# Kernel optimization log

Measured on AMD Instinct MI355X. Metric: run time of the kernel, lower is better.

## Reference

```python
import jax, jax.numpy as jnp
import numpy as np

B, T, H = 262144, 15, 64


def setup_inputs() -> dict:
    key = jax.random.key(0)
    ks = jax.random.split(key, 8)
    s_ih = 1.0 / np.sqrt(H)
    return {
        "x": jax.random.normal(ks[0], (B, T), dtype=jnp.float32),
        # PyTorch GRU params: W_ih [3H, input_size=1], W_hh [3H, H], biases [3H]
        "W_ih": jax.random.uniform(ks[1], (3 * H, 1), jnp.float32, -s_ih, s_ih),
        "W_hh": jax.random.uniform(ks[2], (3 * H, H), jnp.float32, -s_ih, s_ih),
        "b_ih": jax.random.uniform(ks[3], (3 * H,), jnp.float32, -s_ih, s_ih),
        "b_hh": jax.random.uniform(ks[4], (3 * H,), jnp.float32, -s_ih, s_ih),
        "W_fc": jax.random.uniform(ks[5], (2, H), jnp.float32, -s_ih, s_ih),
        "b_fc": jax.random.uniform(ks[6], (2,), jnp.float32, -s_ih, s_ih),
    }


def reference(x, W_ih, W_hh, b_ih, b_hh, W_fc, b_fc):
    # x: [B, T]; each scalar feature is one timestep of a 1-dim GRU input.
    w_in = W_ih[:, 0]  # [3H] since input_size == 1

    def step(h, x_t):
        # x_t: [B]; input gates are just outer product with w_in (input_size=1)
        xg = x_t[:, None] * w_in[None, :] + b_ih          # [B, 3H]
        hg = h @ W_hh.T + b_hh                            # [B, 3H]
        r = jax.nn.sigmoid(xg[:, :H] + hg[:, :H])
        z = jax.nn.sigmoid(xg[:, H:2 * H] + hg[:, H:2 * H])
        n = jnp.tanh(xg[:, 2 * H:] + r * hg[:, 2 * H:])
        h_new = (1.0 - z) * n + z * h
        return h_new, None

    h0 = jnp.zeros((x.shape[0], H), dtype=x.dtype)
    h_last, _ = jax.lax.scan(step, h0, x.T)  # scan over time dim
    logits = h_last @ W_fc.T + b_fc          # [B, 2]
    return logits
```

## Files before the change

kernel.cpp:

```cpp
#include <hip/hip_runtime.h>

#define T_STEPS 15
#define ROWS_PER_BLOCK 64
#define B_TOTAL 262144
#define LOG2E 1.4426950408889634f

typedef _Float16 half8 __attribute__((ext_vector_type(8)));
typedef _Float16 half4 __attribute__((ext_vector_type(4)));
typedef __fp16   fp16x2 __attribute__((ext_vector_type(2)));
typedef float f32x4 __attribute__((ext_vector_type(4)));

#define MFMA_INIT(acc, a, b, cseed) \
    asm("v_mfma_f32_16x16x32_f16 %0, %1, %2, %3" : "=&v"(acc) : "v"(a), "v"(b), "v"(cseed))
#define MFMA_ACC(acc, a, b) \
    asm("v_mfma_f32_16x16x32_f16 %0, %1, %2, %0" : "+v"(acc) : "v"(a), "v"(b))

__device__ __forceinline__ int swz(int row, int e) {
    return (row * 64 + e) ^ ((row & 7) << 3);
}

__global__ __launch_bounds__(256, 3) void gru_mfma_kernel(
    const float* __restrict__ x,
    const float* __restrict__ W_ih,
    const float* __restrict__ W_hh,
    const float* __restrict__ b_ih,
    const float* __restrict__ b_hh,
    const float* __restrict__ W_fc,
    const float* __restrict__ b_fc,
    float* __restrict__ out)
{
    __shared__ _Float16 wlds[192 * 64];
    __shared__ float    xlds[T_STEPS * ROWS_PER_BLOCK];
    __shared__ _Float16 hst[4][2][16 * 64];

    const int tid  = threadIdx.x;
    const int wave = tid >> 6;
    const int lane = tid & 63;
    const int c    = lane & 15;
    const int g4   = lane >> 4;
    const int r0   = blockIdx.x * ROWS_PER_BLOCK;

    for (int idx = tid; idx < 192 * 64; idx += 256) {
        int n = idx >> 6, s = idx & 63;
        int korig = (s & 3) * 16 + (s >> 2);
        float scale = (n < 128) ? LOG2E : (2.0f * LOG2E);
        wlds[swz(n, s)] = (_Float16)(W_hh[n * 64 + korig] * scale);
    }
    for (int idx = tid; idx < ROWS_PER_BLOCK * T_STEPS; idx += 256) {
        int row = idx / T_STEPS, t = idx - row * T_STEPS;
        xlds[t * 64 + row] = x[r0 * T_STEPS + idx];
    }
    __syncthreads();

    float wihr[4], wihz[4], wihn[4], seedn[4], bihn[4];
    f32x4 sr4[4], sz4[4];
#pragma unroll
    for (int tq = 0; tq < 4; ++tq) {
        int jn = tq * 16 + c;
        wihr[tq]  = W_ih[jn] * LOG2E;
        wihz[tq]  = W_ih[64 + jn] * LOG2E;
        wihn[tq]  = W_ih[128 + jn] * (2.0f * LOG2E);
        float sr  = (b_ih[jn] + b_hh[jn]) * LOG2E;
        float sz  = (b_ih[64 + jn] + b_hh[64 + jn]) * LOG2E;
        sr4[tq] = (f32x4){sr, sr, sr, sr};
        sz4[tq] = (f32x4){sz, sz, sz, sz};
        seedn[tq] = b_hh[128 + jn] * (2.0f * LOG2E);
        bihn[tq]  = b_ih[128 + jn] * (2.0f * LOG2E);
    }

    const int eS0 = c * 64 + (((g4 * 8) + 0)  ^ ((c & 7) << 3));
    const int eS1 = c * 64 + (((g4 * 8) + 32) ^ ((c & 7) << 3));
    const int bytesS0 = eS0 * 2;
    const int bytesS1 = eS1 * 2;
    const _Float16* aptr0 = &hst[wave][0][eS0];
    const _Float16* aptr1 = &hst[wave][0][eS1];
    _Float16* wr[4];
#pragma unroll
    for (int reg = 0; reg < 4; ++reg) {
        int row = g4 * 4 + reg;
        wr[reg] = &hst[wave][0][row * 64 + ((c * 4) ^ ((row & 7) << 3))];
    }

    const f32x4 zero4 = (f32x4){0.0f, 0.0f, 0.0f, 0.0f};

    f32x4 accr[4], accz[4], accn[4];
#pragma unroll
    for (int tq = 0; tq < 4; ++tq) {
        accr[tq] = sr4[tq];
        accz[tq] = sz4[tq];
        accn[tq] = zero4;
    }

    float h[4][4];
#pragma unroll
    for (int tq = 0; tq < 4; ++tq)
#pragma unroll
        for (int reg = 0; reg < 4; ++reg) h[tq][reg] = 0.0f;

    const char* wbase = (const char*)&wlds[0];

#pragma unroll 1
    for (int t = 0; t < T_STEPS; ++t) {
        if (t > 0) {
            int ofA = bytesS0, ofB = bytesS1;
            asm volatile("" : "+v"(ofA), "+v"(ofB));
            const char* bp0 = wbase + ofA;
            const char* bp1 = wbase + ofB;

            half8 Ahi0 = *(const half8*)aptr0;
            half8 Ahi1 = *(const half8*)aptr1;
            half8 Alo0 = *(const half8*)(aptr0 + 1024);
            half8 Alo1 = *(const half8*)(aptr1 + 1024);
#pragma unroll
            for (int tq = 0; tq < 4; ++tq) {
                half8 Br0 = *(const half8*)(bp0 + tq * 2048);
                half8 Br1 = *(const half8*)(bp1 + tq * 2048);
                half8 Bz0 = *(const half8*)(bp0 + (4 + tq) * 2048);
                half8 Bz1 = *(const half8*)(bp1 + (4 + tq) * 2048);
                half8 Bn0 = *(const half8*)(bp0 + (8 + tq) * 2048);
                half8 Bn1 = *(const half8*)(bp1 + (8 + tq) * 2048);
                MFMA_INIT(accr[tq], Ahi0, Br0, sr4[tq]);
                MFMA_ACC (accr[tq], Ahi1, Br1);
                MFMA_INIT(accz[tq], Ahi0, Bz0, sz4[tq]);
                MFMA_ACC (accz[tq], Ahi1, Bz1);
                MFMA_INIT(accn[tq], Ahi0, Bn0, zero4);
                MFMA_ACC (accn[tq], Ahi1, Bn1);
                MFMA_ACC (accn[tq], Alo0, Bn0);
                MFMA_ACC (accn[tq], Alo1, Bn1);
                if (tq < 3) __builtin_amdgcn_sched_barrier(0);
            }
            __builtin_amdgcn_sched_barrier(0);
            asm volatile("s_nop 7\n\ts_nop 7");
            __builtin_amdgcn_sched_barrier(0);
        }

        f32x4 xt4 = *(const f32x4*)&xlds[t * 64 + wave * 16 + g4 * 4];

#pragma unroll
        for (int reg = 0; reg < 4; ++reg) {
            float xt = xt4[reg];
            float hnv[4];
#pragma unroll
            for (int tq = 0; tq < 4; ++tq) {
                float pr = __builtin_fmaf(xt, wihr[tq], accr[tq][reg]);
                float er = __builtin_amdgcn_exp2f(-pr);
                float rg = __builtin_amdgcn_rcpf(1.0f + er);
                float pz = __builtin_fmaf(xt, wihz[tq], accz[tq][reg]);
                float ez = __builtin_amdgcn_exp2f(-pz);
                float na2 = __builtin_fmaf(rg, seedn[tq],
                             __builtin_fmaf(xt, wihn[tq], bihn[tq]));
                float na  = __builtin_fmaf(rg, accn[tq][reg], na2);
                float en = __builtin_amdgcn_exp2f(-na);
                float A  = 1.0f + en;
                float Cc = 1.0f + ez;
                float D  = A * Cc;
                float R  = __builtin_amdgcn_rcpf(D);
                float P  = __builtin_fmaf(-en, ez, ez);
                float num = __builtin_fmaf(h[tq][reg], A, P);
                float hn = num * R;
                h[tq][reg] = hn;
                hnv[tq] = hn;
            }
            fp16x2 h01 = __builtin_amdgcn_cvt_pkrtz(hnv[0], hnv[1]);
            fp16x2 h23 = __builtin_amdgcn_cvt_pkrtz(hnv[2], hnv[3]);
            float l0 = hnv[0] - (float)h01[0];
            float l1 = hnv[1] - (float)h01[1];
            float l2 = hnv[2] - (float)h23[0];
            float l3 = hnv[3] - (float)h23[1];
            fp16x2 l01 = __builtin_amdgcn_cvt_pkrtz(l0, l1);
            fp16x2 l23 = __builtin_amdgcn_cvt_pkrtz(l2, l3);
            half4 vh, vl;
            vh[0] = (_Float16)h01[0]; vh[1] = (_Float16)h01[1];
            vh[2] = (_Float16)h23[0]; vh[3] = (_Float16)h23[1];
            vl[0] = (_Float16)l01[0]; vl[1] = (_Float16)l01[1];
            vl[2] = (_Float16)l23[0]; vl[3] = (_Float16)l23[1];
            *(half4*)wr[reg] = vh;
            *(half4*)(wr[reg] + 1024) = vl;
        }
    }

    const float* wfc = W_fc;
    const float* bfc = b_fc;
    asm volatile("" : "+v"(wfc), "+v"(bfc));
    float wfc0[4], wfc1[4];
#pragma unroll
    for (int tq = 0; tq < 4; ++tq) {
        wfc0[tq] = wfc[tq * 16 + c];
        wfc1[tq] = wfc[64 + tq * 16 + c];
    }
#pragma unroll
    for (int reg = 0; reg < 4; ++reg) {
        float s0 = 0.0f, s1 = 0.0f;
#pragma unroll
        for (int tq = 0; tq < 4; ++tq) {
            s0 = __builtin_fmaf(h[tq][reg], wfc0[tq], s0);
            s1 = __builtin_fmaf(h[tq][reg], wfc1[tq], s1);
        }
#pragma unroll
        for (int m = 1; m < 16; m <<= 1) {
            s0 += __shfl_xor(s0, m, 64);
            s1 += __shfl_xor(s1, m, 64);
        }
        if (c == 0) {
            int gr = r0 + wave * 16 + g4 * 4 + reg;
            out[gr * 2 + 0] = s0 + bfc[0];
            out[gr * 2 + 1] = s1 + bfc[1];
        }
    }
}

extern "C" void kernel_launch(void* const* d_in, const int* in_sizes, int n_in,
                              void* d_out, int out_size, void* d_ws, size_t ws_size,
                              hipStream_t stream) {
    const float* x    = (const float*)d_in[0];
    const float* W_ih = (const float*)d_in[1];
    const float* W_hh = (const float*)d_in[2];
    const float* b_ih = (const float*)d_in[3];
    const float* b_hh = (const float*)d_in[4];
    const float* W_fc = (const float*)d_in[5];
    const float* b_fc = (const float*)d_in[6];
    float* out = (float*)d_out;

    dim3 grid(B_TOTAL / ROWS_PER_BLOCK);
    dim3 block(256);
    gru_mfma_kernel<<<grid, block, 0, stream>>>(x, W_ih, W_hh, b_ih, b_hh, W_fc, b_fc, out);
}
```

Baseline: 236.2 us.

## Drop fp16 hi/lo split of hidden state and process two row tiles per wave

Removes the low-part correction for the hidden state, so h is stored in LDS as a single fp16 value and the n-gate no longer needs two extra MFMAs. Each wave now handles two 16-row tiles, with 128 rows per block, so the W_hh B-fragments loaded from LDS are reused across both tiles. Biases are added in the scalar epilogue instead of seeding the MFMA accumulators. Occupancy drops from 3 to 2 blocks per CU, and the lower-precision recurrence may lose accuracy against the fp32 reference.

```diff
diff --git a/kernel.cpp b/kernel.cpp
--- a/kernel.cpp
+++ b/kernel.cpp
@@ -1,7 +1,7 @@
 #include <hip/hip_runtime.h>
 
 #define T_STEPS 15
-#define ROWS_PER_BLOCK 64
+#define ROWS_PER_BLOCK 128
 #define B_TOTAL 262144
 #define LOG2E 1.4426950408889634f
 
@@ -10,8 +10,8 @@
 typedef __fp16   fp16x2 __attribute__((ext_vector_type(2)));
 typedef float f32x4 __attribute__((ext_vector_type(4)));
 
-#define MFMA_INIT(acc, a, b, cseed) \
-    asm("v_mfma_f32_16x16x32_f16 %0, %1, %2, %3" : "=&v"(acc) : "v"(a), "v"(b), "v"(cseed))
+#define MFMA_INIT(acc, a, b, cz) \
+    asm("v_mfma_f32_16x16x32_f16 %0, %1, %2, %3" : "=&v"(acc) : "v"(a), "v"(b), "v"(cz))
 #define MFMA_ACC(acc, a, b) \
     asm("v_mfma_f32_16x16x32_f16 %0, %1, %2, %0" : "+v"(acc) : "v"(a), "v"(b))
 
@@ -19,7 +19,7 @@
     return (row * 64 + e) ^ ((row & 7) << 3);
 }
 
-__global__ __launch_bounds__(256, 3) void gru_mfma_kernel(
+__global__ __launch_bounds__(256, 2) void gru_mfma_kernel(
     const float* __restrict__ x,
     const float* __restrict__ W_ih,
     const float* __restrict__ W_hh,
@@ -31,7 +31,7 @@
 {
     __shared__ _Float16 wlds[192 * 64];
     __shared__ float    xlds[T_STEPS * ROWS_PER_BLOCK];
-    __shared__ _Float16 hst[4][2][16 * 64];
+    __shared__ _Float16 hst[8][16 * 64];
 
     const int tid  = threadIdx.x;
     const int wave = tid >> 6;
@@ -48,22 +48,19 @@
     }
     for (int idx = tid; idx < ROWS_PER_BLOCK * T_STEPS; idx += 256) {
         int row = idx / T_STEPS, t = idx - row * T_STEPS;
-        xlds[t * 64 + row] = x[r0 * T_STEPS + idx];
+        xlds[t * ROWS_PER_BLOCK + row] = x[r0 * T_STEPS + idx];
     }
     __syncthreads();
 
-    float wihr[4], wihz[4], wihn[4], seedn[4], bihn[4];
-    f32x4 sr4[4], sz4[4];
+    float wihr[4], wihz[4], wihn[4], sr[4], sz[4], seedn[4], bihn[4];
 #pragma unroll
     for (int tq = 0; tq < 4; ++tq) {
         int jn = tq * 16 + c;
         wihr[tq]  = W_ih[jn] * LOG2E;
         wihz[tq]  = W_ih[64 + jn] * LOG2E;
         wihn[tq]  = W_ih[128 + jn] * (2.0f * LOG2E);
-        float sr  = (b_ih[jn] + b_hh[jn]) * LOG2E;
-        float sz  = (b_ih[64 + jn] + b_hh[64 + jn]) * LOG2E;
-        sr4[tq] = (f32x4){sr, sr, sr, sr};
-        sz4[tq] = (f32x4){sz, sz, sz, sz};
+        sr[tq]    = (b_ih[jn] + b_hh[jn]) * LOG2E;
+        sz[tq]    = (b_ih[64 + jn] + b_hh[64 + jn]) * LOG2E;
         seedn[tq] = b_hh[128 + jn] * (2.0f * LOG2E);
         bihn[tq]  = b_ih[128 + jn] * (2.0f * LOG2E);
     }
@@ -72,30 +69,38 @@
     const int eS1 = c * 64 + (((g4 * 8) + 32) ^ ((c & 7) << 3));
     const int bytesS0 = eS0 * 2;
     const int bytesS1 = eS1 * 2;
-    const _Float16* aptr0 = &hst[wave][0][eS0];
-    const _Float16* aptr1 = &hst[wave][0][eS1];
-    _Float16* wr[4];
-#pragma unroll
-    for (int reg = 0; reg < 4; ++reg) {
-        int row = g4 * 4 + reg;
-        wr[reg] = &hst[wave][0][row * 64 + ((c * 4) ^ ((row & 7) << 3))];
-    }
+    const _Float16* aA0 = &hst[wave * 2 + 0][eS0];
+    const _Float16* aA1 = &hst[wave * 2 + 0][eS1];
+    const _Float16* aB0 = &hst[wave * 2 + 1][eS0];
+    const _Float16* aB1 = &hst[wave * 2 + 1][eS1];
+    _Float16* wr[2][4];
+#pragma unroll
+    for (int s = 0; s < 2; ++s)
+#pragma unroll
+        for (int reg = 0; reg < 4; ++reg) {
+            int row = g4 * 4 + reg;
+            wr[s][reg] = &hst[wave * 2 + s][row * 64 + ((c * 4) ^ ((row & 7) << 3))];
+        }
 
     const f32x4 zero4 = (f32x4){0.0f, 0.0f, 0.0f, 0.0f};
 
-    f32x4 accr[4], accz[4], accn[4];
-#pragma unroll
-    for (int tq = 0; tq < 4; ++tq) {
-        accr[tq] = sr4[tq];
-        accz[tq] = sz4[tq];
-        accn[tq] = zero4;
-    }
-
-    float h[4][4];
-#pragma unroll
-    for (int tq = 0; tq < 4; ++tq)
-#pragma unroll
-        for (int reg = 0; reg < 4; ++reg) h[tq][reg] = 0.0f;
+    f32x4 accr[2][4], accz[2][4], accn[2][4];
+#pragma unroll
+    for (int s = 0; s < 2; ++s)
+#pragma unroll
+        for (int tq = 0; tq < 4; ++tq) {
+            accr[s][tq] = zero4;
+            accz[s][tq] = zero4;
+            accn[s][tq] = zero4;
+        }
+
+    float h[2][4][4];
+#pragma unroll
+    for (int s = 0; s < 2; ++s)
+#pragma unroll
+        for (int tq = 0; tq < 4; ++tq)
+#pragma unroll
+            for (int reg = 0; reg < 4; ++reg) h[s][tq][reg] = 0.0f;
 
     const char* wbase = (const char*)&wlds[0];
 
@@ -107,10 +112,10 @@
             const char* bp0 = wbase + ofA;
             const char* bp1 = wbase + ofB;
 
-            half8 Ahi0 = *(const half8*)aptr0;
-            half8 Ahi1 = *(const half8*)aptr1;
-            half8 Alo0 = *(const half8*)(aptr0 + 1024);
-            half8 Alo1 = *(const half8*)(aptr1 + 1024);
+            half8 A0sA = *(const half8*)aA0;
+            half8 A1sA = *(const half8*)aA1;
+            half8 A0sB = *(const half8*)aB0;
+            half8 A1sB = *(const half8*)aB1;
 #pragma unroll
             for (int tq = 0; tq < 4; ++tq) {
                 half8 Br0 = *(const half8*)(bp0 + tq * 2048);
@@ -119,14 +124,18 @@
                 half8 Bz1 = *(const half8*)(bp1 + (4 + tq) * 2048);
                 half8 Bn0 = *(const half8*)(bp0 + (8 + tq) * 2048);
                 half8 Bn1 = *(const half8*)(bp1 + (8 + tq) * 2048);
-                MFMA_INIT(accr[tq], Ahi0, Br0, sr4[tq]);
-                MFMA_ACC (accr[tq], Ahi1, Br1);
-                MFMA_INIT(accz[tq], Ahi0, Bz0, sz4[tq]);
-                MFMA_ACC (accz[tq], Ahi1, Bz1);
-                MFMA_INIT(accn[tq], Ahi0, Bn0, zero4);
-                MFMA_ACC (accn[tq], Ahi1, Bn1);
-                MFMA_ACC (accn[tq], Alo0, Bn0);
-                MFMA_ACC (accn[tq], Alo1, Bn1);
+                MFMA_INIT(accr[0][tq], A0sA, Br0, zero4);
+                MFMA_ACC (accr[0][tq], A1sA, Br1);
+                MFMA_INIT(accz[0][tq], A0sA, Bz0, zero4);
+                MFMA_ACC (accz[0][tq], A1sA, Bz1);
+                MFMA_INIT(accn[0][tq], A0sA, Bn0, zero4);
+                MFMA_ACC (accn[0][tq], A1sA, Bn1);
+                MFMA_INIT(accr[1][tq], A0sB, Br0, zero4);
+                MFMA_ACC (accr[1][tq], A1sB, Br1);
+                MFMA_INIT(accz[1][tq], A0sB, Bz0, zero4);
+                MFMA_ACC (accz[1][tq], A1sB, Bz1);
+                MFMA_INIT(accn[1][tq], A0sB, Bn0, zero4);
+                MFMA_ACC (accn[1][tq], A1sB, Bn1);
                 if (tq < 3) __builtin_amdgcn_sched_barrier(0);
             }
             __builtin_amdgcn_sched_barrier(0);
@@ -134,48 +143,41 @@
             __builtin_amdgcn_sched_barrier(0);
         }
 
-        f32x4 xt4 = *(const f32x4*)&xlds[t * 64 + wave * 16 + g4 * 4];
-
-#pragma unroll
-        for (int reg = 0; reg < 4; ++reg) {
-            float xt = xt4[reg];
-            float hnv[4];
-#pragma unroll
-            for (int tq = 0; tq < 4; ++tq) {
-                float pr = __builtin_fmaf(xt, wihr[tq], accr[tq][reg]);
-                float er = __builtin_amdgcn_exp2f(-pr);
-                float rg = __builtin_amdgcn_rcpf(1.0f + er);
-                float pz = __builtin_fmaf(xt, wihz[tq], accz[tq][reg]);
-                float ez = __builtin_amdgcn_exp2f(-pz);
-                float na2 = __builtin_fmaf(rg, seedn[tq],
-                             __builtin_fmaf(xt, wihn[tq], bihn[tq]));
-                float na  = __builtin_fmaf(rg, accn[tq][reg], na2);
-                float en = __builtin_amdgcn_exp2f(-na);
-                float A  = 1.0f + en;
-                float Cc = 1.0f + ez;
-                float D  = A * Cc;
-                float R  = __builtin_amdgcn_rcpf(D);
-                float P  = __builtin_fmaf(-en, ez, ez);
-                float num = __builtin_fmaf(h[tq][reg], A, P);
-                float hn = num * R;
-                h[tq][reg] = hn;
-                hnv[tq] = hn;
+#pragma unroll
+        for (int s = 0; s < 2; ++s) {
+            f32x4 xt4 = *(const f32x4*)&xlds[t * ROWS_PER_BLOCK + wave * 32 + s * 16 + g4 * 4];
+#pragma unroll
+            for (int reg = 0; reg < 4; ++reg) {
+                float xt = xt4[reg];
+                float hnv[4];
+#pragma unroll
+                for (int tq = 0; tq < 4; ++tq) {
+                    float pr = accr[s][tq][reg] + __builtin_fmaf(xt, wihr[tq], sr[tq]);
+                    float er = __builtin_amdgcn_exp2f(-pr);
+                    float rg = __builtin_amdgcn_rcpf(1.0f + er);
+                    float pz = accz[s][tq][reg] + __builtin_fmaf(xt, wihz[tq], sz[tq]);
+                    float ez = __builtin_amdgcn_exp2f(-pz);
+                    float na = __builtin_fmaf(rg, accn[s][tq][reg],
+                                __builtin_fmaf(rg, seedn[tq],
+                                 __builtin_fmaf(xt, wihn[tq], bihn[tq])));
+                    float en = __builtin_amdgcn_exp2f(-na);
+                    float A  = 1.0f + en;
+                    float Cc = 1.0f + ez;
+                    float D  = A * Cc;
+                    float R  = __builtin_amdgcn_rcpf(D);
+                    float P  = __builtin_fmaf(-en, ez, ez);
+                    float num = __builtin_fmaf(h[s][tq][reg], A, P);
+                    float hn = num * R;
+                    h[s][tq][reg] = hn;
+                    hnv[tq] = hn;
+                }
+                fp16x2 h01 = __builtin_amdgcn_cvt_pkrtz(hnv[0], hnv[1]);
+                fp16x2 h23 = __builtin_amdgcn_cvt_pkrtz(hnv[2], hnv[3]);
+                half4 vh;
+                vh[0] = (_Float16)h01[0]; vh[1] = (_Float16)h01[1];
+                vh[2] = (_Float16)h23[0]; vh[3] = (_Float16)h23[1];
+                *(half4*)wr[s][reg] = vh;
             }
-            fp16x2 h01 = __builtin_amdgcn_cvt_pkrtz(hnv[0], hnv[1]);
-            fp16x2 h23 = __builtin_amdgcn_cvt_pkrtz(hnv[2], hnv[3]);
-            float l0 = hnv[0] - (float)h01[0];
-            float l1 = hnv[1] - (float)h01[1];
-            float l2 = hnv[2] - (float)h23[0];
-            float l3 = hnv[3] - (float)h23[1];
-            fp16x2 l01 = __builtin_amdgcn_cvt_pkrtz(l0, l1);
-            fp16x2 l23 = __builtin_amdgcn_cvt_pkrtz(l2, l3);
-            half4 vh, vl;
-            vh[0] = (_Float16)h01[0]; vh[1] = (_Float16)h01[1];
-            vh[2] = (_Float16)h23[0]; vh[3] = (_Float16)h23[1];
-            vl[0] = (_Float16)l01[0]; vl[1] = (_Float16)l01[1];
-            vl[2] = (_Float16)l23[0]; vl[3] = (_Float16)l23[1];
-            *(half4*)wr[reg] = vh;
-            *(half4*)(wr[reg] + 1024) = vl;
         }
     }
 
@@ -189,12 +191,14 @@
         wfc1[tq] = wfc[64 + tq * 16 + c];
     }
 #pragma unroll
+    for (int s = 0; s < 2; ++s)
+#pragma unroll
     for (int reg = 0; reg < 4; ++reg) {
         float s0 = 0.0f, s1 = 0.0f;
 #pragma unroll
         for (int tq = 0; tq < 4; ++tq) {
-            s0 = __builtin_fmaf(h[tq][reg], wfc0[tq], s0);
-            s1 = __builtin_fmaf(h[tq][reg], wfc1[tq], s1);
+            s0 = __builtin_fmaf(h[s][tq][reg], wfc0[tq], s0);
+            s1 = __builtin_fmaf(h[s][tq][reg], wfc1[tq], s1);
         }
 #pragma unroll
         for (int m = 1; m < 16; m <<= 1) {
@@ -202,7 +206,7 @@
             s1 += __shfl_xor(s1, m, 64);
         }
         if (c == 0) {
-            int gr = r0 + wave * 16 + g4 * 4 + reg;
+            int gr = r0 + wave * 32 + s * 16 + g4 * 4 + reg;
             out[gr * 2 + 0] = s0 + bfc[0];
             out[gr * 2 + 1] = s1 + bfc[1];
         }
```

Result: faster. 215.9 us (-8.6%).
